# Optimization experiments

Measured on AMD Instinct MI355X. Metric: run time of the kernel, lower is better.

Reference implementation:

```python
import jax, jax.numpy as jnp
import numpy as np

B, S, D = 2, 2048, 2048
NH, NKV, HD = 32, 8, 64
ROPE_BASE = 10000.0


def rope(x):
    # x: [b, s, h, d]; torchtune-style interleaved-pair RoPE
    b, s, h, d = x.shape
    pos = jnp.arange(s, dtype=jnp.float32)
    inv_freq = 1.0 / (ROPE_BASE ** (jnp.arange(0, d, 2, dtype=jnp.float32) / d))
    ang = pos[:, None] * inv_freq[None, :]            # [s, d//2]
    cos = jnp.cos(ang)[None, :, None, :].astype(x.dtype)
    sin = jnp.sin(ang)[None, :, None, :].astype(x.dtype)
    xr = x.reshape(b, s, h, d // 2, 2)
    x0, x1 = xr[..., 0], xr[..., 1]
    out = jnp.stack([x0 * cos - x1 * sin, x0 * sin + x1 * cos], axis=-1)
    return out.reshape(b, s, h, d)


def setup_inputs() -> dict:
    key = jax.random.key(0)
    ks = jax.random.split(key, 5)
    return {
        "x": jax.random.normal(ks[0], (B, S, D), dtype=jnp.float32),
        "Wq": jax.random.normal(ks[1], (NH * HD, D), dtype=jnp.float32) * 0.02,
        "Wk": jax.random.normal(ks[2], (NKV * HD, D), dtype=jnp.float32) * 0.02,
        "Wv": jax.random.normal(ks[3], (NKV * HD, D), dtype=jnp.float32) * 0.02,
        "Wo": jax.random.normal(ks[4], (D, NH * HD), dtype=jnp.float32) * 0.02,
    }


def reference(x, Wq, Wk, Wv, Wo):
    b, s, _ = x.shape
    qpk = NH // NKV  # queries per kv head
    # projections (Linear, no bias)
    q = (x @ Wq.T).reshape(b, s, NH, HD)
    k = (x @ Wk.T).reshape(b, s, NKV, HD)
    v = (x @ Wv.T).reshape(b, s, NKV, HD)
    # RoPE on q and k (expanding k before RoPE == RoPE on kv heads then group-broadcast)
    q = rope(q)
    k = rope(k)
    # grouped attention: q -> [b, s, g, n, d], k/v stay [b, s, g, d]
    qg = q.reshape(b, s, NKV, qpk, HD)
    scale = 1.0 / jnp.sqrt(jnp.array(HD, dtype=x.dtype))
    scores = jnp.einsum("bqgnd,bkgd->bgnqk", qg, k) * scale  # [b,g,n,s,s]
    attn = jax.nn.softmax(scores, axis=-1)
    out = jnp.einsum("bgnqk,bkgd->bqgnd", attn, v)           # [b,s,g,n,d]
    out = out.reshape(b, s, NH * HD)
    return out @ Wo.T
```

## Files before the change

### kernel.cpp

```cpp
#include <hip/hip_runtime.h>
#include <hip/hip_bf16.h>
#include <math.h>

#define SLEN 2048
#define DMODEL 2048
#define NH 32
#define NKV 8
#define HD 64
#define BATCH 2
#define MROWS (BATCH * SLEN)
#define QKVN (NH * HD + 2 * NKV * HD)

typedef __attribute__((ext_vector_type(8))) short bf16x8;
typedef __attribute__((ext_vector_type(4))) float f32x4;
typedef __attribute__((ext_vector_type(16))) float f32x16;
typedef __attribute__((ext_vector_type(4))) unsigned u32x4;

__device__ __forceinline__ unsigned short f2bf(float f) {
  union { float f; unsigned u; } v; v.f = f;
  return (unsigned short)((v.u + 0x7FFFu + ((v.u >> 16) & 1u)) >> 16);
}
__device__ __forceinline__ float bf2f(unsigned short h) {
  union { unsigned u; float f; } v; v.u = ((unsigned)h) << 16;
  return v.f;
}
__device__ __forceinline__ unsigned cvt_pk_bf16(float lo, float hi) {
  unsigned r;
  asm("v_cvt_pk_bf16_f32 %0, %1, %2" : "=v"(r) : "v"(lo), "v"(hi));
  return r;
}
__device__ __forceinline__ float fast_exp2(float x) {
#if __has_builtin(__builtin_amdgcn_exp2f)
  return __builtin_amdgcn_exp2f(x);
#else
  return exp2f(x);
#endif
}
__device__ __forceinline__ void fast_sincos(float ang, float* sn, float* cs) {
#if __has_builtin(__builtin_amdgcn_sinf) && __has_builtin(__builtin_amdgcn_cosf)
  float rev = ang * 0.15915494309189535f;
#if __has_builtin(__builtin_amdgcn_fractf)
  rev = __builtin_amdgcn_fractf(rev);
#else
  rev = rev - floorf(rev);
#endif
  *sn = __builtin_amdgcn_sinf(rev);
  *cs = __builtin_amdgcn_cosf(rev);
#else
  sincosf(ang, sn, cs);
#endif
}
__device__ __forceinline__ float red32_add(float x) {
  float a = x, b;
  asm volatile("v_mov_b32 %0, %1" : "=v"(b) : "v"(x));
  asm volatile("v_permlane32_swap_b32 %0, %1" : "+v"(a), "+v"(b));
  return a + b;
}
__device__ __forceinline__ void gload_lds16(const unsigned short* g, unsigned short* l) {
  __builtin_amdgcn_global_load_lds(
      (const __attribute__((address_space(1))) unsigned int*)(g),
      (__attribute__((address_space(3))) unsigned int*)(l), 16, 0, 0);
}

__global__ __launch_bounds__(256) void cvt_all_kernel(
    const float* __restrict__ x,
    const float* __restrict__ Wq, const float* __restrict__ Wk,
    const float* __restrict__ Wv, const float* __restrict__ Wo,
    unsigned short* __restrict__ xb, unsigned short* __restrict__ wqkvb,
    unsigned short* __restrict__ wob) {
  const int i = blockIdx.x * 256 + threadIdx.x;
  const float* src;
  unsigned short* dst;
  size_t off;
  if (i < 1048576)      { src = x;  dst = xb;              off = i; }
  else if (i < 1572864) { src = Wq; dst = wqkvb;           off = i - 1048576; }
  else if (i < 1703936) { src = Wk; dst = wqkvb + 4194304; off = i - 1572864; }
  else if (i < 1835008) { src = Wv; dst = wqkvb + 5242880; off = i - 1703936; }
  else                  { src = Wo; dst = wob;             off = i - 1835008; }
  const float4 a = *(const float4*)&src[off * 8];
  const float4 b = *(const float4*)&src[off * 8 + 4];
  uint4 o;
  o.x = cvt_pk_bf16(a.x, a.y);
  o.y = cvt_pk_bf16(a.z, a.w);
  o.z = cvt_pk_bf16(b.x, b.y);
  o.w = cvt_pk_bf16(b.z, b.w);
  *(uint4*)&dst[off * 8] = o;
}

template <int OUTBF16>
__global__ __launch_bounds__(256) void gemm_bf16_kernel(
    const unsigned short* __restrict__ A, const unsigned short* __restrict__ B,
    void* __restrict__ Cv, int M, int N, int K) {
  __shared__ unsigned short As[128][32];
  __shared__ unsigned short Bs[128][32];

  const int tid = threadIdx.x;
  const int lane = tid & 63;
  const int wid = tid >> 6;
  const int g = lane >> 4;
  const int fr = lane & 15;
  const int m0 = blockIdx.x * 128;
  const int n0 = blockIdx.y * 128;
  const int wm = (wid >> 1) * 64;
  const int wn = (wid & 1) * 64;

  const int srow = wid * 32 + (lane >> 2);
  const int scol = (lane & 3) * 8;
  const unsigned short* ga = &A[(size_t)(m0 + srow) * K + scol];
  const unsigned short* gb = &B[(size_t)(n0 + srow) * K + scol];
  unsigned short* la0 = &As[wid * 32][0];
  unsigned short* la1 = &As[wid * 32 + 16][0];
  unsigned short* lb0 = &Bs[wid * 32][0];
  unsigned short* lb1 = &Bs[wid * 32 + 16][0];
  const size_t rstep = (size_t)16 * K;

  f32x4 acc[4][4];
#pragma unroll
  for (int i = 0; i < 4; i++)
#pragma unroll
    for (int j = 0; j < 4; j++) acc[i][j] = (f32x4){0.f, 0.f, 0.f, 0.f};

  for (int kt = 0; kt < K; kt += 32) {
    __syncthreads();
    gload_lds16(ga + kt, la0);
    gload_lds16(ga + kt + rstep, la1);
    gload_lds16(gb + kt, lb0);
    gload_lds16(gb + kt + rstep, lb1);
    __syncthreads();

    bf16x8 af[4], bfr[4];
#pragma unroll
    for (int i = 0; i < 4; i++) {
      af[i] = *(const bf16x8*)&As[wm + i * 16 + fr][g * 8];
      bfr[i] = *(const bf16x8*)&Bs[wn + i * 16 + fr][g * 8];
    }
#pragma unroll
    for (int i = 0; i < 4; i++)
#pragma unroll
      for (int j = 0; j < 4; j++)
        acc[i][j] = __builtin_amdgcn_mfma_f32_16x16x32_bf16(af[i], bfr[j], acc[i][j], 0, 0, 0);
  }

  if constexpr (OUTBF16) {
    unsigned short* C = (unsigned short*)Cv;
#pragma unroll
    for (int i = 0; i < 4; i++)
#pragma unroll
      for (int j = 0; j < 4; j++)
#pragma unroll
        for (int r = 0; r < 4; r++)
          C[(size_t)(m0 + wm + i * 16 + g * 4 + r) * N + n0 + wn + j * 16 + fr] =
              f2bf(acc[i][j][r]);
  } else {
    float* C = (float*)Cv;
#pragma unroll
    for (int i = 0; i < 4; i++)
#pragma unroll
      for (int j = 0; j < 4; j++)
#pragma unroll
        for (int r = 0; r < 4; r++)
          C[(size_t)(m0 + wm + i * 16 + g * 4 + r) * N + n0 + wn + j * 16 + fr] =
              acc[i][j][r];
  }
}

__global__ __launch_bounds__(256) void kv_prep_kernel(const unsigned short* __restrict__ qkvb,
                                                      unsigned short* __restrict__ kb,
                                                      unsigned short* __restrict__ vt) {
  __shared__ unsigned short tile[64][72];
  const int bi = blockIdx.x;
  const int tid = threadIdx.x;
  if (bi < 4096) {
    const int idx = bi * 256 + tid;
    const int j = idx & 31;
    const int s = (idx >> 5) & (SLEN - 1);
    const int kh = (idx >> 16) & (NKV - 1);
    const int b = idx >> 19;
    const unsigned pin =
        *(const unsigned*)&qkvb[(size_t)(b * SLEN + s) * QKVN + NH * HD + kh * HD + 2 * j];
    const float x0 = bf2f((unsigned short)(pin & 0xffffu));
    const float x1 = bf2f((unsigned short)(pin >> 16));
    const float inv = fast_exp2(-0.20762050593f * (float)(2 * j));
    float sn, cs;
    fast_sincos((float)s * inv, &sn, &cs);
    const float o0 = x0 * cs - x1 * sn;
    const float o1 = x0 * sn + x1 * cs;
    *(unsigned*)&kb[((size_t)(b * NKV + kh) * SLEN + s) * HD + 2 * j] = cvt_pk_bf16(o0, o1);
  } else {
    const int bv = bi - 4096;
    const int st = bv & 31;
    const int kh = (bv >> 5) & 7;
    const int b = bv >> 8;
    const int r = tid >> 2;
    const int c0 = (tid & 3) * 16;
    const unsigned short* src =
        &qkvb[(size_t)(b * SLEN + st * 64 + r) * QKVN + (NH + NKV) * HD + kh * HD + c0];
    *(bf16x8*)&tile[r][c0] = *(const bf16x8*)src;
    *(bf16x8*)&tile[r][c0 + 8] = *(const bf16x8*)(src + 8);
    __syncthreads();
    alignas(16) unsigned short tmp[16];
#pragma unroll
    for (int i = 0; i < 16; ++i) tmp[i] = tile[c0 + i][r];
    unsigned short* dst = &vt[((size_t)(b * NKV + kh) * HD + r) * SLEN + st * 64 + c0];
    *(bf16x8*)dst = *(bf16x8*)tmp;
    *(bf16x8*)(dst + 8) = *(bf16x8*)(tmp + 8);
  }
}

__global__ __launch_bounds__(512) void attn_kernel(
    const unsigned short* __restrict__ qkvb, const unsigned short* __restrict__ kb,
    const unsigned short* __restrict__ vt, unsigned short* __restrict__ aob) {
  __shared__ unsigned short Kbuf[2][4096];
  __shared__ unsigned short Vbuf[2][4096];

  const int tid = threadIdx.x;
  const int lane = tid & 63;
  const int wid = tid >> 6;
  const int lq = lane & 31;
  const int hi = lane >> 5;
  const int sw = lane & 7;

  const int jb = blockIdx.x;
  const int xcd = jb & 7;
  const int idx = jb >> 3;
  const int bh = xcd * 8 + (idx & 7);
  const int qt = idx >> 3;
  const int b = bh >> 5, h = bh & 31;
  const int kh = h >> 2;
  const size_t kbase = (size_t)(b * NKV + kh) * SLEN * HD;
  const size_t vbase = (size_t)(b * NKV + kh) * HD * SLEN;

  const int q0 = qt * 256 + wid * 32;
  const int s = q0 + lq;
  const unsigned short* qsrc = &qkvb[(size_t)(b * SLEN + s) * QKVN + h * HD];
  bf16x8 qf[4];
#pragma unroll
  for (int ks = 0; ks < 4; ++ks) {
    const bf16x8 raw = *(const bf16x8*)(qsrc + ks * 16 + hi * 8);
    unsigned pk[4];
#pragma unroll
    for (int p = 0; p < 4; ++p) {
      const int j = ks * 8 + hi * 4 + p;
      const float inv = fast_exp2(-0.20762050593f * (float)(2 * j));
      float sn, cs;
      fast_sincos((float)s * inv, &sn, &cs);
      const float SC = 0.18033688011f;
      const float x0 = bf2f((unsigned short)raw[2 * p]);
      const float x1 = bf2f((unsigned short)raw[2 * p + 1]);
      pk[p] = cvt_pk_bf16((x0 * cs - x1 * sn) * SC, (x0 * sn + x1 * cs) * SC);
    }
    u32x4 t = {pk[0], pk[1], pk[2], pk[3]};
    qf[ks] = __builtin_bit_cast(bf16x8, t);
  }

  const int swzc = ((lane & 7) ^ ((lane >> 3) & 7)) * 8;
  const int srow = wid * 8 + (lane >> 3);
  const unsigned short* gk0 = kb + kbase + (size_t)srow * HD + swzc;
  const unsigned short* gv0 = vt + vbase + (size_t)srow * SLEN + swzc;

  f32x16 acc0 = {}, acc1 = {};
  float lacc = 0.f;

  gload_lds16(gk0, &Kbuf[0][wid * 512]);
  gload_lds16(gv0, &Vbuf[0][wid * 512]);

  for (int kt = 0; kt < SLEN / 64; ++kt) {
    const int cur = kt & 1;
    asm volatile("s_waitcnt vmcnt(0)" ::: "memory");
    __syncthreads();
    if (kt + 1 < SLEN / 64) {
      const int nxt = cur ^ 1;
      const size_t ko = (size_t)(kt + 1) * 64 * HD;
      const size_t vo = (size_t)(kt + 1) * 64;
      gload_lds16(gk0 + ko, &Kbuf[nxt][wid * 512]);
      gload_lds16(gv0 + vo, &Vbuf[nxt][wid * 512]);
    }

    f32x16 s0 = {}, s1 = {};
#pragma unroll
    for (int ks = 0; ks < 4; ++ks) {
      const bf16x8 kf = *(const bf16x8*)&Kbuf[cur][lq * HD + (((ks * 2 + hi) ^ sw) * 8)];
      s0 = __builtin_amdgcn_mfma_f32_32x32x16_bf16(kf, qf[ks], s0, 0, 0, 0);
    }
#pragma unroll
    for (int ks = 0; ks < 4; ++ks) {
      const bf16x8 kf = *(const bf16x8*)&Kbuf[cur][(32 + lq) * HD + (((ks * 2 + hi) ^ sw) * 8)];
      s1 = __builtin_amdgcn_mfma_f32_32x32x16_bf16(kf, qf[ks], s1, 0, 0, 0);
    }

    float p0[16], p1[16];
#pragma unroll
    for (int i = 0; i < 16; ++i) p0[i] = fast_exp2(s0[i]);
#pragma unroll
    for (int i = 0; i < 16; ++i) p1[i] = fast_exp2(s1[i]);
    float ls0 = 0.f, ls1 = 0.f, ls2 = 0.f, ls3 = 0.f;
#pragma unroll
    for (int i = 0; i < 4; ++i) {
      ls0 += p0[i]; ls1 += p0[i + 4]; ls2 += p0[i + 8]; ls3 += p0[i + 12];
    }
#pragma unroll
    for (int i = 0; i < 4; ++i) {
      ls0 += p1[i]; ls1 += p1[i + 4]; ls2 += p1[i + 8]; ls3 += p1[i + 12];
    }
    lacc += (ls0 + ls1) + (ls2 + ls3);

    unsigned u0[8], u1[8];
#pragma unroll
    for (int c = 0; c < 4; ++c) {
      u0[2 * c] = cvt_pk_bf16(p0[4 * c], p0[4 * c + 1]);
      u0[2 * c + 1] = cvt_pk_bf16(p0[4 * c + 2], p0[4 * c + 3]);
      u1[2 * c] = cvt_pk_bf16(p1[4 * c], p1[4 * c + 1]);
      u1[2 * c + 1] = cvt_pk_bf16(p1[4 * c + 2], p1[4 * c + 3]);
    }
    bf16x8 pf[4];
    {
      unsigned a0 = u0[0], b0 = u0[2];
      asm volatile("v_permlane32_swap_b32 %0, %1" : "+v"(a0), "+v"(b0));
      unsigned a1 = u0[1], b1 = u0[3];
      asm volatile("v_permlane32_swap_b32 %0, %1" : "+v"(a1), "+v"(b1));
      u32x4 t = {a0, a1, b0, b1};
      pf[0] = __builtin_bit_cast(bf16x8, t);
      unsigned a2 = u0[4], b2 = u0[6];
      asm volatile("v_permlane32_swap_b32 %0, %1" : "+v"(a2), "+v"(b2));
      unsigned a3 = u0[5], b3 = u0[7];
      asm volatile("v_permlane32_swap_b32 %0, %1" : "+v"(a3), "+v"(b3));
      u32x4 t2 = {a2, a3, b2, b3};
      pf[1] = __builtin_bit_cast(bf16x8, t2);
      unsigned a4 = u1[0], b4 = u1[2];
      asm volatile("v_permlane32_swap_b32 %0, %1" : "+v"(a4), "+v"(b4));
      unsigned a5 = u1[1], b5 = u1[3];
      asm volatile("v_permlane32_swap_b32 %0, %1" : "+v"(a5), "+v"(b5));
      u32x4 t3 = {a4, a5, b4, b5};
      pf[2] = __builtin_bit_cast(bf16x8, t3);
      unsigned a6 = u1[4], b6 = u1[6];
      asm volatile("v_permlane32_swap_b32 %0, %1" : "+v"(a6), "+v"(b6));
      unsigned a7 = u1[5], b7 = u1[7];
      asm volatile("v_permlane32_swap_b32 %0, %1" : "+v"(a7), "+v"(b7));
      u32x4 t4 = {a6, a7, b6, b7};
      pf[3] = __builtin_bit_cast(bf16x8, t4);
    }

#pragma unroll
    for (int ks = 0; ks < 4; ++ks) {
      const bf16x8 vf = *(const bf16x8*)&Vbuf[cur][lq * 64 + (((ks * 2 + hi) ^ sw) * 8)];
      acc0 = __builtin_amdgcn_mfma_f32_32x32x16_bf16(vf, pf[ks], acc0, 0, 0, 0);
    }
#pragma unroll
    for (int ks = 0; ks < 4; ++ks) {
      const bf16x8 vf = *(const bf16x8*)&Vbuf[cur][(32 + lq) * 64 + (((ks * 2 + hi) ^ sw) * 8)];
      acc1 = __builtin_amdgcn_mfma_f32_32x32x16_bf16(vf, pf[ks], acc1, 0, 0, 0);
    }
  }

  const float l = red32_add(lacc);
  const float rl = 1.0f / l;
  const size_t obase = (size_t)(b * SLEN + q0 + lq) * DMODEL + h * HD;
#pragma unroll
  for (int c = 0; c < 4; ++c) {
    uint2 o;
    o.x = cvt_pk_bf16(acc0[4 * c] * rl, acc0[4 * c + 1] * rl);
    o.y = cvt_pk_bf16(acc0[4 * c + 2] * rl, acc0[4 * c + 3] * rl);
    *(uint2*)&aob[obase + 8 * c + 4 * hi] = o;
    uint2 o2;
    o2.x = cvt_pk_bf16(acc1[4 * c] * rl, acc1[4 * c + 1] * rl);
    o2.y = cvt_pk_bf16(acc1[4 * c + 2] * rl, acc1[4 * c + 3] * rl);
    *(uint2*)&aob[obase + 32 + 8 * c + 4 * hi] = o2;
  }
}

extern "C" void kernel_launch(void* const* d_in, const int* in_sizes, int n_in,
                              void* d_out, int out_size, void* d_ws, size_t ws_size,
                              hipStream_t stream) {
  const float* x  = (const float*)d_in[0];
  const float* Wq = (const float*)d_in[1];
  const float* Wk = (const float*)d_in[2];
  const float* Wv = (const float*)d_in[3];
  const float* Wo = (const float*)d_in[4];
  float* out = (float*)d_out;

  char* ws = (char*)d_ws;
  unsigned short* qkvb = (unsigned short*)ws; ws += (size_t)MROWS * QKVN * 2;
  unsigned short* kb = (unsigned short*)ws;   ws += (size_t)BATCH * NKV * SLEN * HD * 2;
  unsigned short* vt = (unsigned short*)ws;   ws += (size_t)BATCH * NKV * HD * SLEN * 2;
  unsigned short* xb = (unsigned short*)ws;   ws += (size_t)MROWS * DMODEL * 2;
  unsigned short* aob = xb;
  unsigned short* wqkvb = (unsigned short*)ws; ws += (size_t)QKVN * DMODEL * 2;
  unsigned short* wob = (unsigned short*)ws;

  dim3 blk(256);

  cvt_all_kernel<<<9216, blk, 0, stream>>>(x, Wq, Wk, Wv, Wo, xb, wqkvb, wob);

  gemm_bf16_kernel<1><<<dim3(MROWS / 128, QKVN / 128), blk, 0, stream>>>(
      xb, wqkvb, qkvb, MROWS, QKVN, DMODEL);

  kv_prep_kernel<<<4608, blk, 0, stream>>>(qkvb, kb, vt);

  attn_kernel<<<dim3(512), dim3(512), 0, stream>>>(qkvb, kb, vt, aob);

  gemm_bf16_kernel<0><<<dim3(MROWS / 128, DMODEL / 128), blk, 0, stream>>>(
      aob, wob, out, MROWS, DMODEL, DMODEL);
}
```

Baseline: 221.4 us.

## Double KV tile to 128 keys per barrier with new LDS swizzle

Raises the attention kernel's K/V staging tile from 64 to 128 keys per iteration. This halves the number of s_waitcnt/__syncthreads barriers and double-buffer swaps, and the inner loop now processes two 64-key halves per staged tile. It also adds a new XOR swizzle for K rows and for the wider 128-column V-transposed rows to avoid LDS bank conflicts. LDS use doubles to 64 KB per block, which may limit occupancy, and each wave now issues four async loads per stage.

```diff
diff --git a/kernel.cpp b/kernel.cpp
--- a/kernel.cpp
+++ b/kernel.cpp
@@ -210,15 +210,15 @@
 __global__ __launch_bounds__(512) void attn_kernel(
     const unsigned short* __restrict__ qkvb, const unsigned short* __restrict__ kb,
     const unsigned short* __restrict__ vt, unsigned short* __restrict__ aob) {
-  __shared__ unsigned short Kbuf[2][4096];
-  __shared__ unsigned short Vbuf[2][4096];
+  __shared__ unsigned short Kbuf[2][128 * 64];
+  __shared__ unsigned short Vbuf[2][64 * 128];
 
   const int tid = threadIdx.x;
   const int lane = tid & 63;
   const int wid = tid >> 6;
   const int lq = lane & 31;
   const int hi = lane >> 5;
-  const int sw = lane & 7;
+  const int f0 = (lane & 7) ^ (lq >> 3);
 
   const int jb = blockIdx.x;
   const int xcd = jb & 7;
@@ -253,102 +253,120 @@
     qf[ks] = __builtin_bit_cast(bf16x8, t);
   }
 
-  const int swzc = ((lane & 7) ^ ((lane >> 3) & 7)) * 8;
-  const int srow = wid * 8 + (lane >> 3);
-  const unsigned short* gk0 = kb + kbase + (size_t)srow * HD + swzc;
-  const unsigned short* gv0 = vt + vbase + (size_t)srow * SLEN + swzc;
+  const int cgA = (lane & 7) ^ (((lane >> 3) ^ (2 * wid)) & 7);
+  const int rowA = 16 * wid + (lane >> 3);
+  const unsigned short* gkA = kb + kbase + (size_t)rowA * HD + cgA * 8;
+  const unsigned short* gkB = kb + kbase + (size_t)(rowA + 8) * HD + (cgA ^ 1) * 8;
+  const int cgC = (lane & 15) ^ (((lane >> 4) ^ wid) & 7);
+  const int rowC = 8 * wid + (lane >> 4);
+  const unsigned short* gvC = vt + vbase + (size_t)rowC * SLEN + cgC * 8;
+  const unsigned short* gvD = vt + vbase + (size_t)(rowC + 4) * SLEN + (cgC ^ 4) * 8;
 
   f32x16 acc0 = {}, acc1 = {};
   float lacc = 0.f;
 
-  gload_lds16(gk0, &Kbuf[0][wid * 512]);
-  gload_lds16(gv0, &Vbuf[0][wid * 512]);
-
-  for (int kt = 0; kt < SLEN / 64; ++kt) {
+  gload_lds16(gkA, &Kbuf[0][16 * wid * 64]);
+  gload_lds16(gkB, &Kbuf[0][(16 * wid + 8) * 64]);
+  gload_lds16(gvC, &Vbuf[0][8 * wid * 128]);
+  gload_lds16(gvD, &Vbuf[0][(8 * wid + 4) * 128]);
+
+  for (int kt = 0; kt < SLEN / 128; ++kt) {
     const int cur = kt & 1;
     asm volatile("s_waitcnt vmcnt(0)" ::: "memory");
     __syncthreads();
-    if (kt + 1 < SLEN / 64) {
+    if (kt + 1 < SLEN / 128) {
       const int nxt = cur ^ 1;
-      const size_t ko = (size_t)(kt + 1) * 64 * HD;
-      const size_t vo = (size_t)(kt + 1) * 64;
-      gload_lds16(gk0 + ko, &Kbuf[nxt][wid * 512]);
-      gload_lds16(gv0 + vo, &Vbuf[nxt][wid * 512]);
+      const size_t ko = (size_t)(kt + 1) * 128 * HD;
+      const size_t vo = (size_t)(kt + 1) * 128;
+      gload_lds16(gkA + ko, &Kbuf[nxt][16 * wid * 64]);
+      gload_lds16(gkB + ko, &Kbuf[nxt][(16 * wid + 8) * 64]);
+      gload_lds16(gvC + vo, &Vbuf[nxt][8 * wid * 128]);
+      gload_lds16(gvD + vo, &Vbuf[nxt][(8 * wid + 4) * 128]);
     }
 
-    f32x16 s0 = {}, s1 = {};
-#pragma unroll
-    for (int ks = 0; ks < 4; ++ks) {
-      const bf16x8 kf = *(const bf16x8*)&Kbuf[cur][lq * HD + (((ks * 2 + hi) ^ sw) * 8)];
-      s0 = __builtin_amdgcn_mfma_f32_32x32x16_bf16(kf, qf[ks], s0, 0, 0, 0);
-    }
-#pragma unroll
-    for (int ks = 0; ks < 4; ++ks) {
-      const bf16x8 kf = *(const bf16x8*)&Kbuf[cur][(32 + lq) * HD + (((ks * 2 + hi) ^ sw) * 8)];
-      s1 = __builtin_amdgcn_mfma_f32_32x32x16_bf16(kf, qf[ks], s1, 0, 0, 0);
-    }
-
-    float p0[16], p1[16];
-#pragma unroll
-    for (int i = 0; i < 16; ++i) p0[i] = fast_exp2(s0[i]);
-#pragma unroll
-    for (int i = 0; i < 16; ++i) p1[i] = fast_exp2(s1[i]);
-    float ls0 = 0.f, ls1 = 0.f, ls2 = 0.f, ls3 = 0.f;
-#pragma unroll
-    for (int i = 0; i < 4; ++i) {
-      ls0 += p0[i]; ls1 += p0[i + 4]; ls2 += p0[i + 8]; ls3 += p0[i + 12];
-    }
-#pragma unroll
-    for (int i = 0; i < 4; ++i) {
-      ls0 += p1[i]; ls1 += p1[i + 4]; ls2 += p1[i + 8]; ls3 += p1[i + 12];
-    }
-    lacc += (ls0 + ls1) + (ls2 + ls3);
-
-    unsigned u0[8], u1[8];
-#pragma unroll
-    for (int c = 0; c < 4; ++c) {
-      u0[2 * c] = cvt_pk_bf16(p0[4 * c], p0[4 * c + 1]);
-      u0[2 * c + 1] = cvt_pk_bf16(p0[4 * c + 2], p0[4 * c + 3]);
-      u1[2 * c] = cvt_pk_bf16(p1[4 * c], p1[4 * c + 1]);
-      u1[2 * c + 1] = cvt_pk_bf16(p1[4 * c + 2], p1[4 * c + 3]);
-    }
-    bf16x8 pf[4];
-    {
-      unsigned a0 = u0[0], b0 = u0[2];
-      asm volatile("v_permlane32_swap_b32 %0, %1" : "+v"(a0), "+v"(b0));
-      unsigned a1 = u0[1], b1 = u0[3];
-      asm volatile("v_permlane32_swap_b32 %0, %1" : "+v"(a1), "+v"(b1));
-      u32x4 t = {a0, a1, b0, b1};
-      pf[0] = __builtin_bit_cast(bf16x8, t);
-      unsigned a2 = u0[4], b2 = u0[6];
-      asm volatile("v_permlane32_swap_b32 %0, %1" : "+v"(a2), "+v"(b2));
-      unsigned a3 = u0[5], b3 = u0[7];
-      asm volatile("v_permlane32_swap_b32 %0, %1" : "+v"(a3), "+v"(b3));
-      u32x4 t2 = {a2, a3, b2, b3};
-      pf[1] = __builtin_bit_cast(bf16x8, t2);
-      unsigned a4 = u1[0], b4 = u1[2];
-      asm volatile("v_permlane32_swap_b32 %0, %1" : "+v"(a4), "+v"(b4));
-      unsigned a5 = u1[1], b5 = u1[3];
-      asm volatile("v_permlane32_swap_b32 %0, %1" : "+v"(a5), "+v"(b5));
-      u32x4 t3 = {a4, a5, b4, b5};
-      pf[2] = __builtin_bit_cast(bf16x8, t3);
-      unsigned a6 = u1[4], b6 = u1[6];
-      asm volatile("v_permlane32_swap_b32 %0, %1" : "+v"(a6), "+v"(b6));
-      unsigned a7 = u1[5], b7 = u1[7];
-      asm volatile("v_permlane32_swap_b32 %0, %1" : "+v"(a7), "+v"(b7));
-      u32x4 t4 = {a6, a7, b6, b7};
-      pf[3] = __builtin_bit_cast(bf16x8, t4);
-    }
-
-#pragma unroll
-    for (int ks = 0; ks < 4; ++ks) {
-      const bf16x8 vf = *(const bf16x8*)&Vbuf[cur][lq * 64 + (((ks * 2 + hi) ^ sw) * 8)];
-      acc0 = __builtin_amdgcn_mfma_f32_32x32x16_bf16(vf, pf[ks], acc0, 0, 0, 0);
-    }
-#pragma unroll
-    for (int ks = 0; ks < 4; ++ks) {
-      const bf16x8 vf = *(const bf16x8*)&Vbuf[cur][(32 + lq) * 64 + (((ks * 2 + hi) ^ sw) * 8)];
-      acc1 = __builtin_amdgcn_mfma_f32_32x32x16_bf16(vf, pf[ks], acc1, 0, 0, 0);
+#pragma unroll
+    for (int half = 0; half < 2; ++half) {
+      const int rb = half * 64;
+
+      f32x16 s0 = {}, s1 = {};
+#pragma unroll
+      for (int ks = 0; ks < 4; ++ks) {
+        const bf16x8 kf =
+            *(const bf16x8*)&Kbuf[cur][(rb + lq) * 64 + ((ks * 2 + hi) ^ f0) * 8];
+        s0 = __builtin_amdgcn_mfma_f32_32x32x16_bf16(kf, qf[ks], s0, 0, 0, 0);
+      }
+#pragma unroll
+      for (int ks = 0; ks < 4; ++ks) {
+        const bf16x8 kf =
+            *(const bf16x8*)&Kbuf[cur][(rb + 32 + lq) * 64 + ((ks * 2 + hi) ^ f0 ^ 4) * 8];
+        s1 = __builtin_amdgcn_mfma_f32_32x32x16_bf16(kf, qf[ks], s1, 0, 0, 0);
+      }
+
+      float p0[16], p1[16];
+#pragma unroll
+      for (int i = 0; i < 16; ++i) p0[i] = fast_exp2(s0[i]);
+#pragma unroll
+      for (int i = 0; i < 16; ++i) p1[i] = fast_exp2(s1[i]);
+      float ls0 = 0.f, ls1 = 0.f, ls2 = 0.f, ls3 = 0.f;
+#pragma unroll
+      for (int i = 0; i < 4; ++i) {
+        ls0 += p0[i]; ls1 += p0[i + 4]; ls2 += p0[i + 8]; ls3 += p0[i + 12];
+      }
+#pragma unroll
+      for (int i = 0; i < 4; ++i) {
+        ls0 += p1[i]; ls1 += p1[i + 4]; ls2 += p1[i + 8]; ls3 += p1[i + 12];
+      }
+      lacc += (ls0 + ls1) + (ls2 + ls3);
+
+      unsigned u0[8], u1[8];
+#pragma unroll
+      for (int c = 0; c < 4; ++c) {
+        u0[2 * c] = cvt_pk_bf16(p0[4 * c], p0[4 * c + 1]);
+        u0[2 * c + 1] = cvt_pk_bf16(p0[4 * c + 2], p0[4 * c + 3]);
+        u1[2 * c] = cvt_pk_bf16(p1[4 * c], p1[4 * c + 1]);
+        u1[2 * c + 1] = cvt_pk_bf16(p1[4 * c + 2], p1[4 * c + 3]);
+      }
+      bf16x8 pf[4];
+      {
+        unsigned a0 = u0[0], b0 = u0[2];
+        asm volatile("v_permlane32_swap_b32 %0, %1" : "+v"(a0), "+v"(b0));
+        unsigned a1 = u0[1], b1 = u0[3];
+        asm volatile("v_permlane32_swap_b32 %0, %1" : "+v"(a1), "+v"(b1));
+        u32x4 t = {a0, a1, b0, b1};
+        pf[0] = __builtin_bit_cast(bf16x8, t);
+        unsigned a2 = u0[4], b2 = u0[6];
+        asm volatile("v_permlane32_swap_b32 %0, %1" : "+v"(a2), "+v"(b2));
+        unsigned a3 = u0[5], b3 = u0[7];
+        asm volatile("v_permlane32_swap_b32 %0, %1" : "+v"(a3), "+v"(b3));
+        u32x4 t2 = {a2, a3, b2, b3};
+        pf[1] = __builtin_bit_cast(bf16x8, t2);
+        unsigned a4 = u1[0], b4 = u1[2];
+        asm volatile("v_permlane32_swap_b32 %0, %1" : "+v"(a4), "+v"(b4));
+        unsigned a5 = u1[1], b5 = u1[3];
+        asm volatile("v_permlane32_swap_b32 %0, %1" : "+v"(a5), "+v"(b5));
+        u32x4 t3 = {a4, a5, b4, b5};
+        pf[2] = __builtin_bit_cast(bf16x8, t3);
+        unsigned a6 = u1[4], b6 = u1[6];
+        asm volatile("v_permlane32_swap_b32 %0, %1" : "+v"(a6), "+v"(b6));
+        unsigned a7 = u1[5], b7 = u1[7];
+        asm volatile("v_permlane32_swap_b32 %0, %1" : "+v"(a7), "+v"(b7));
+        u32x4 t4 = {a6, a7, b6, b7};
+        pf[3] = __builtin_bit_cast(bf16x8, t4);
+      }
+
+#pragma unroll
+      for (int ks = 0; ks < 4; ++ks) {
+        const bf16x8 vf =
+            *(const bf16x8*)&Vbuf[cur][lq * 128 + (half * 8 + ((ks * 2 + hi) ^ f0)) * 8];
+        acc0 = __builtin_amdgcn_mfma_f32_32x32x16_bf16(vf, pf[ks], acc0, 0, 0, 0);
+      }
+#pragma unroll
+      for (int ks = 0; ks < 4; ++ks) {
+        const bf16x8 vf =
+            *(const bf16x8*)&Vbuf[cur][(32 + lq) * 128 +
+                                       (half * 8 + ((ks * 2 + hi) ^ f0 ^ 4)) * 8];
+        acc1 = __builtin_amdgcn_mfma_f32_32x32x16_bf16(vf, pf[ks], acc1, 0, 0, 0);
+      }
     }
   }
 
```

Measured after the change: 225.8 us. Within noise of the previous version (+2.0%).

## Triple-buffer K/V tiles and change LDS swizzle to cut bank conflicts

Applied to the files above, without the earlier changes.

Moves the attention K/V staging from double to triple buffering in LDS. The next tile's global-to-LDS load is now issued before the wait, and the wait uses vmcnt(2), so the load overlaps the current tile's compute. The XOR swizzle also changes to fold in the wave id and a per-half offset, aiming to reduce LDS bank conflicts on the MFMA operand reads. It adds a third buffer's worth of LDS, which may lower occupancy, and the compute body becomes a macro with the last iteration peeled off.

```diff
diff --git a/kernel.cpp b/kernel.cpp
--- a/kernel.cpp
+++ b/kernel.cpp
@@ -210,15 +210,15 @@
 __global__ __launch_bounds__(512) void attn_kernel(
     const unsigned short* __restrict__ qkvb, const unsigned short* __restrict__ kb,
     const unsigned short* __restrict__ vt, unsigned short* __restrict__ aob) {
-  __shared__ unsigned short Kbuf[2][4096];
-  __shared__ unsigned short Vbuf[2][4096];
+  __shared__ unsigned short Kbuf[3][4096];
+  __shared__ unsigned short Vbuf[3][4096];
 
   const int tid = threadIdx.x;
   const int lane = tid & 63;
   const int wid = tid >> 6;
   const int lq = lane & 31;
   const int hi = lane >> 5;
-  const int sw = lane & 7;
+  const int f0 = (lq & 7) ^ (lq >> 3);
 
   const int jb = blockIdx.x;
   const int xcd = jb & 7;
@@ -253,7 +253,7 @@
     qf[ks] = __builtin_bit_cast(bf16x8, t);
   }
 
-  const int swzc = ((lane & 7) ^ ((lane >> 3) & 7)) * 8;
+  const int swzc = (((lane & 7) ^ (lane >> 3) ^ wid) & 7) * 8;
   const int srow = wid * 8 + (lane >> 3);
   const unsigned short* gk0 = kb + kbase + (size_t)srow * HD + swzc;
   const unsigned short* gv0 = vt + vbase + (size_t)srow * SLEN + swzc;
@@ -264,93 +264,90 @@
   gload_lds16(gk0, &Kbuf[0][wid * 512]);
   gload_lds16(gv0, &Vbuf[0][wid * 512]);
 
-  for (int kt = 0; kt < SLEN / 64; ++kt) {
-    const int cur = kt & 1;
-    asm volatile("s_waitcnt vmcnt(0)" ::: "memory");
+#define ATTN_COMPUTE(CUR)                                                              \
+  {                                                                                    \
+    f32x16 s0 = {}, s1 = {};                                                           \
+    _Pragma("unroll") for (int ks = 0; ks < 4; ++ks) {                                 \
+      const bf16x8 kf =                                                                \
+          *(const bf16x8*)&Kbuf[CUR][lq * 64 + (((ks * 2 + hi) ^ f0) * 8)];            \
+      s0 = __builtin_amdgcn_mfma_f32_32x32x16_bf16(kf, qf[ks], s0, 0, 0, 0);           \
+    }                                                                                  \
+    _Pragma("unroll") for (int ks = 0; ks < 4; ++ks) {                                 \
+      const bf16x8 kf =                                                                \
+          *(const bf16x8*)&Kbuf[CUR][(32 + lq) * 64 + (((ks * 2 + hi) ^ f0 ^ 4) * 8)]; \
+      s1 = __builtin_amdgcn_mfma_f32_32x32x16_bf16(kf, qf[ks], s1, 0, 0, 0);           \
+    }                                                                                  \
+    float p0[16], p1[16];                                                              \
+    _Pragma("unroll") for (int i = 0; i < 16; ++i) p0[i] = fast_exp2(s0[i]);           \
+    _Pragma("unroll") for (int i = 0; i < 16; ++i) p1[i] = fast_exp2(s1[i]);           \
+    float ls0 = 0.f, ls1 = 0.f, ls2 = 0.f, ls3 = 0.f;                                  \
+    _Pragma("unroll") for (int i = 0; i < 4; ++i) {                                    \
+      ls0 += p0[i]; ls1 += p0[i + 4]; ls2 += p0[i + 8]; ls3 += p0[i + 12];             \
+    }                                                                                  \
+    _Pragma("unroll") for (int i = 0; i < 4; ++i) {                                    \
+      ls0 += p1[i]; ls1 += p1[i + 4]; ls2 += p1[i + 8]; ls3 += p1[i + 12];             \
+    }                                                                                  \
+    lacc += (ls0 + ls1) + (ls2 + ls3);                                                 \
+    unsigned u0[8], u1[8];                                                             \
+    _Pragma("unroll") for (int c = 0; c < 4; ++c) {                                    \
+      u0[2 * c] = cvt_pk_bf16(p0[4 * c], p0[4 * c + 1]);                               \
+      u0[2 * c + 1] = cvt_pk_bf16(p0[4 * c + 2], p0[4 * c + 3]);                       \
+      u1[2 * c] = cvt_pk_bf16(p1[4 * c], p1[4 * c + 1]);                               \
+      u1[2 * c + 1] = cvt_pk_bf16(p1[4 * c + 2], p1[4 * c + 3]);                       \
+    }                                                                                  \
+    bf16x8 pf[4];                                                                      \
+    {                                                                                  \
+      unsigned a0 = u0[0], b0 = u0[2];                                                 \
+      asm volatile("v_permlane32_swap_b32 %0, %1" : "+v"(a0), "+v"(b0));               \
+      unsigned a1 = u0[1], b1 = u0[3];                                                 \
+      asm volatile("v_permlane32_swap_b32 %0, %1" : "+v"(a1), "+v"(b1));               \
+      u32x4 t = {a0, a1, b0, b1};                                                      \
+      pf[0] = __builtin_bit_cast(bf16x8, t);                                           \
+      unsigned a2 = u0[4], b2 = u0[6];                                                 \
+      asm volatile("v_permlane32_swap_b32 %0, %1" : "+v"(a2), "+v"(b2));               \
+      unsigned a3 = u0[5], b3 = u0[7];                                                 \
+      asm volatile("v_permlane32_swap_b32 %0, %1" : "+v"(a3), "+v"(b3));               \
+      u32x4 t2 = {a2, a3, b2, b3};                                                     \
+      pf[1] = __builtin_bit_cast(bf16x8, t2);                                          \
+      unsigned a4 = u1[0], b4 = u1[2];                                                 \
+      asm volatile("v_permlane32_swap_b32 %0, %1" : "+v"(a4), "+v"(b4));               \
+      unsigned a5 = u1[1], b5 = u1[3];                                                 \
+      asm volatile("v_permlane32_swap_b32 %0, %1" : "+v"(a5), "+v"(b5));               \
+      u32x4 t3 = {a4, a5, b4, b5};                                                     \
+      pf[2] = __builtin_bit_cast(bf16x8, t3);                                          \
+      unsigned a6 = u1[4], b6 = u1[6];                                                 \
+      asm volatile("v_permlane32_swap_b32 %0, %1" : "+v"(a6), "+v"(b6));               \
+      unsigned a7 = u1[5], b7 = u1[7];                                                 \
+      asm volatile("v_permlane32_swap_b32 %0, %1" : "+v"(a7), "+v"(b7));               \
+      u32x4 t4 = {a6, a7, b6, b7};                                                     \
+      pf[3] = __builtin_bit_cast(bf16x8, t4);                                          \
+    }                                                                                  \
+    _Pragma("unroll") for (int ks = 0; ks < 4; ++ks) {                                 \
+      const bf16x8 vf =                                                                \
+          *(const bf16x8*)&Vbuf[CUR][lq * 64 + (((ks * 2 + hi) ^ f0) * 8)];            \
+      acc0 = __builtin_amdgcn_mfma_f32_32x32x16_bf16(vf, pf[ks], acc0, 0, 0, 0);       \
+    }                                                                                  \
+    _Pragma("unroll") for (int ks = 0; ks < 4; ++ks) {                                 \
+      const bf16x8 vf =                                                                \
+          *(const bf16x8*)&Vbuf[CUR][(32 + lq) * 64 + (((ks * 2 + hi) ^ f0 ^ 4) * 8)]; \
+      acc1 = __builtin_amdgcn_mfma_f32_32x32x16_bf16(vf, pf[ks], acc1, 0, 0, 0);       \
+    }                                                                                  \
+  }
+
+  int cur = 0, nxt = 1;
+  for (int kt = 0; kt < SLEN / 64 - 1; ++kt) {
+    gload_lds16(gk0 + (size_t)(kt + 1) * 64 * HD, &Kbuf[nxt][wid * 512]);
+    gload_lds16(gv0 + (size_t)(kt + 1) * 64, &Vbuf[nxt][wid * 512]);
+    asm volatile("s_waitcnt vmcnt(2)" ::: "memory");
     __syncthreads();
-    if (kt + 1 < SLEN / 64) {
-      const int nxt = cur ^ 1;
-      const size_t ko = (size_t)(kt + 1) * 64 * HD;
-      const size_t vo = (size_t)(kt + 1) * 64;
-      gload_lds16(gk0 + ko, &Kbuf[nxt][wid * 512]);
-      gload_lds16(gv0 + vo, &Vbuf[nxt][wid * 512]);
-    }
-
-    f32x16 s0 = {}, s1 = {};
-#pragma unroll
-    for (int ks = 0; ks < 4; ++ks) {
-      const bf16x8 kf = *(const bf16x8*)&Kbuf[cur][lq * HD + (((ks * 2 + hi) ^ sw) * 8)];
-      s0 = __builtin_amdgcn_mfma_f32_32x32x16_bf16(kf, qf[ks], s0, 0, 0, 0);
-    }
-#pragma unroll
-    for (int ks = 0; ks < 4; ++ks) {
-      const bf16x8 kf = *(const bf16x8*)&Kbuf[cur][(32 + lq) * HD + (((ks * 2 + hi) ^ sw) * 8)];
-      s1 = __builtin_amdgcn_mfma_f32_32x32x16_bf16(kf, qf[ks], s1, 0, 0, 0);
-    }
-
-    float p0[16], p1[16];
-#pragma unroll
-    for (int i = 0; i < 16; ++i) p0[i] = fast_exp2(s0[i]);
-#pragma unroll
-    for (int i = 0; i < 16; ++i) p1[i] = fast_exp2(s1[i]);
-    float ls0 = 0.f, ls1 = 0.f, ls2 = 0.f, ls3 = 0.f;
-#pragma unroll
-    for (int i = 0; i < 4; ++i) {
-      ls0 += p0[i]; ls1 += p0[i + 4]; ls2 += p0[i + 8]; ls3 += p0[i + 12];
-    }
-#pragma unroll
-    for (int i = 0; i < 4; ++i) {
-      ls0 += p1[i]; ls1 += p1[i + 4]; ls2 += p1[i + 8]; ls3 += p1[i + 12];
-    }
-    lacc += (ls0 + ls1) + (ls2 + ls3);
-
-    unsigned u0[8], u1[8];
-#pragma unroll
-    for (int c = 0; c < 4; ++c) {
-      u0[2 * c] = cvt_pk_bf16(p0[4 * c], p0[4 * c + 1]);
-      u0[2 * c + 1] = cvt_pk_bf16(p0[4 * c + 2], p0[4 * c + 3]);
-      u1[2 * c] = cvt_pk_bf16(p1[4 * c], p1[4 * c + 1]);
-      u1[2 * c + 1] = cvt_pk_bf16(p1[4 * c + 2], p1[4 * c + 3]);
-    }
-    bf16x8 pf[4];
-    {
-      unsigned a0 = u0[0], b0 = u0[2];
-      asm volatile("v_permlane32_swap_b32 %0, %1" : "+v"(a0), "+v"(b0));
-      unsigned a1 = u0[1], b1 = u0[3];
-      asm volatile("v_permlane32_swap_b32 %0, %1" : "+v"(a1), "+v"(b1));
-      u32x4 t = {a0, a1, b0, b1};
-      pf[0] = __builtin_bit_cast(bf16x8, t);
-      unsigned a2 = u0[4], b2 = u0[6];
-      asm volatile("v_permlane32_swap_b32 %0, %1" : "+v"(a2), "+v"(b2));
-      unsigned a3 = u0[5], b3 = u0[7];
-      asm volatile("v_permlane32_swap_b32 %0, %1" : "+v"(a3), "+v"(b3));
-      u32x4 t2 = {a2, a3, b2, b3};
-      pf[1] = __builtin_bit_cast(bf16x8, t2);
-      unsigned a4 = u1[0], b4 = u1[2];
-      asm volatile("v_permlane32_swap_b32 %0, %1" : "+v"(a4), "+v"(b4));
-      unsigned a5 = u1[1], b5 = u1[3];
-      asm volatile("v_permlane32_swap_b32 %0, %1" : "+v"(a5), "+v"(b5));
-      u32x4 t3 = {a4, a5, b4, b5};
-      pf[2] = __builtin_bit_cast(bf16x8, t3);
-      unsigned a6 = u1[4], b6 = u1[6];
-      asm volatile("v_permlane32_swap_b32 %0, %1" : "+v"(a6), "+v"(b6));
-      unsigned a7 = u1[5], b7 = u1[7];
-      asm volatile("v_permlane32_swap_b32 %0, %1" : "+v"(a7), "+v"(b7));
-      u32x4 t4 = {a6, a7, b6, b7};
-      pf[3] = __builtin_bit_cast(bf16x8, t4);
-    }
-
-#pragma unroll
-    for (int ks = 0; ks < 4; ++ks) {
-      const bf16x8 vf = *(const bf16x8*)&Vbuf[cur][lq * 64 + (((ks * 2 + hi) ^ sw) * 8)];
-      acc0 = __builtin_amdgcn_mfma_f32_32x32x16_bf16(vf, pf[ks], acc0, 0, 0, 0);
-    }
-#pragma unroll
-    for (int ks = 0; ks < 4; ++ks) {
-      const bf16x8 vf = *(const bf16x8*)&Vbuf[cur][(32 + lq) * 64 + (((ks * 2 + hi) ^ sw) * 8)];
-      acc1 = __builtin_amdgcn_mfma_f32_32x32x16_bf16(vf, pf[ks], acc1, 0, 0, 0);
-    }
-  }
+    ATTN_COMPUTE(cur);
+    cur = nxt;
+    nxt = (nxt == 2) ? 0 : nxt + 1;
+  }
+  asm volatile("s_waitcnt vmcnt(0)" ::: "memory");
+  __syncthreads();
+  ATTN_COMPUTE(cur);
+#undef ATTN_COMPUTE
 
   const float l = red32_add(lacc);
   const float rl = 1.0f / l;
```

New measurement: 224.0 us. Within noise of the previous version (+1.1%).
